# Optimization experiments

Hardware: AMD Instinct MI355X
Metric: run time of the kernel (lower is better)

The kernel has to match this reference:

```python
import jax, jax.numpy as jnp
import numpy as np

N_X = 32640   # total xlmr subword tokens (64 seqs x 510 tokens)
N_S = 16320   # total stanza word tokens (2 subwords per word)
E = 65280     # dependency edges (bidirectional, avg degree ~4)
D = 768
GCN_DIM = 256
GCN_NUM = 2
POS_DIM = 4
N_UPOS = 17
N_LABEL = 5


def setup_inputs() -> dict:
    key = jax.random.key(0)
    ks = jax.random.split(key, 8)
    x = jax.random.normal(ks[0], (N_X, D), dtype=jnp.float32)
    # mapStanza2Xlmr as segment ids: xlmr token j belongs to stanza word j//2
    seg = jnp.arange(N_X, dtype=jnp.int32) // 2
    edge_index = jax.random.randint(ks[1], (2, E), 0, N_S, dtype=jnp.int32)
    upos_ids = jax.random.randint(ks[2], (N_S,), 0, N_UPOS, dtype=jnp.int32)
    Wc = jax.random.normal(ks[3], (D, GCN_DIM), dtype=jnp.float32) * 0.02
    bc = jnp.zeros((GCN_DIM,), dtype=jnp.float32)
    gcn_W = jax.random.normal(ks[4], (GCN_NUM, GCN_DIM, GCN_DIM), dtype=jnp.float32) * 0.05
    gcn_b = jnp.zeros((GCN_NUM, GCN_DIM), dtype=jnp.float32)
    upos_table = jax.random.normal(ks[5], (N_UPOS, POS_DIM), dtype=jnp.float32)
    Wcls = jax.random.normal(ks[6], (D + GCN_DIM + POS_DIM, N_LABEL), dtype=jnp.float32) * 0.02
    bcls = jnp.zeros((N_LABEL,), dtype=jnp.float32)
    return {"x": x, "seg": seg, "edge_index": edge_index, "upos_ids": upos_ids,
            "Wc": Wc, "bc": bc, "gcn_W": gcn_W, "gcn_b": gcn_b,
            "upos_table": upos_table, "Wcls": Wcls, "bcls": bcls}


def _gcn_conv(h, srcs, dsts, W, b, n):
    # PyG GCNConv: h' = D^-1/2 (A+I) D^-1/2 (h W) + b  (self loops already in srcs/dsts)
    h = h @ W
    deg = jax.ops.segment_sum(jnp.ones_like(dsts, h.dtype), dsts, num_segments=n)
    dinv = jax.lax.rsqrt(deg)  # deg >= 1 because of self loops
    coef = dinv[srcs] * dinv[dsts]
    out = jax.ops.segment_sum(h[srcs] * coef[:, None], dsts, num_segments=n)
    return out + b


def reference(x, seg, edge_index, upos_ids, Wc, bc, gcn_W, gcn_b, upos_table, Wcls, bcls):
    # mapStanza2Xlmr: mean-pool subword embeddings into stanza word embeddings
    cnt = jax.ops.segment_sum(jnp.ones((N_X,), x.dtype), seg, num_segments=N_S)
    stanza = jax.ops.segment_sum(x, seg, num_segments=N_S) / cnt[:, None]  # [N_S, D]
    # GCN over dependency edges (gcn_mode=0: biedges)
    h = stanza @ Wc + bc
    self_idx = jnp.arange(N_S, dtype=edge_index.dtype)
    srcs = jnp.concatenate([edge_index[0], self_idx])
    dsts = jnp.concatenate([edge_index[1], self_idx])
    for i in range(GCN_NUM):
        h = jax.nn.relu(_gcn_conv(h, srcs, dsts, gcn_W[i], gcn_b[i], N_S))
    # POS embedding + concat + relu
    pos = upos_table[upos_ids]                                  # [N_S, POS_DIM]
    info = jax.nn.relu(jnp.concatenate([h, pos], axis=1))       # [N_S, GCN_DIM+POS_DIM]
    # mapXlmr2Stanza: each subword gathers its (single) word's info
    append = info[seg]                                          # [N_X, GCN_DIM+POS_DIM]
    tok = jnp.concatenate([x, append], axis=1)                  # [N_X, 1028]
    logits = jax.nn.relu(tok) @ Wcls + bcls
    return jax.nn.log_softmax(logits, axis=1)
```

## Files before the change

### kernel.cpp

```cpp
#include <hip/hip_runtime.h>

#define NXT 32640
#define NS  16320
#define NE  65280
#define DD  768
#define GD  256
#define NLAB 5
#define CAP 32

typedef __attribute__((ext_vector_type(8))) short bf16x8;
typedef __attribute__((ext_vector_type(4))) float f32x4;

__device__ inline unsigned short f2b(float f) {
    unsigned int u = __float_as_uint(f);
    unsigned int r = (u + 0x7FFFu + ((u >> 16) & 1u)) >> 16;
    return (unsigned short)r;
}
__device__ inline float b2f(unsigned short h) {
    return __uint_as_float((unsigned int)h << 16);
}

__global__ void k_setup(int* __restrict__ cnt,
                        const float* __restrict__ Wc, unsigned short* __restrict__ WcT,
                        const float* __restrict__ gcn_W, unsigned short* __restrict__ WT,
                        const float* __restrict__ Wcls, float* __restrict__ WclsT) {
    int b = blockIdx.x, t = threadIdx.x;
    if (b < 64) {
        int i = b * 256 + t;
        if (i < NS) cnt[i] = 0;
    } else if (b < 832) {
        int idx = (b - 64) * 256 + t;
        int k = idx / GD, n = idx - k * GD;
        WcT[(size_t)n * DD + k] = f2b(Wc[idx]);
    } else if (b < 1344) {
        int l = (b < 1088) ? 0 : 1;
        int idx = (b - (l ? 1088 : 832)) * 256 + t;
        int k = idx / GD, n = idx - k * GD;
        WT[(size_t)l * GD * GD + (size_t)n * GD + k] = f2b(gcn_W[(size_t)l * GD * GD + idx]);
    } else {
        int idx = (b - 1344) * 256 + t;
        if (idx < NLAB * DD) {
            int l = idx / DD, k = idx - l * DD;
            WclsT[idx] = Wcls[(size_t)k * NLAB + l];
        }
    }
}

__global__ void k_fill(const int* __restrict__ ei, int* __restrict__ cnt,
                       int* __restrict__ csr_src) {
    int e = blockIdx.x * 256 + threadIdx.x;
    if (e < NE) {
        int dst = ei[NE + e];
        int slot = atomicAdd(&cnt[dst], 1);
        if (slot < CAP) csr_src[(size_t)dst * CAP + slot] = ei[e];
    }
}

__global__ __launch_bounds__(256) void k_xpass(const float* __restrict__ x,
                                               const float* __restrict__ WclsT,
                                               float* __restrict__ partial,
                                               unsigned short* __restrict__ stanza) {
    int w    = blockIdx.x * 4 + (threadIdx.x >> 6);
    int lane = threadIdx.x & 63;
    const float* xr0 = x + (size_t)(2 * w) * DD + lane * 4;
    const float* xr1 = xr0 + DD;
    f32x4 a[3], b[3];
#pragma unroll
    for (int p = 0; p < 3; ++p) {
        a[p] = *(const f32x4*)(xr0 + p * 256);
        b[p] = *(const f32x4*)(xr1 + p * 256);
    }
#pragma unroll
    for (int p = 0; p < 3; ++p) {
        ushort4 o;
        o.x = f2b((a[p][0] + b[p][0]) * 0.5f);
        o.y = f2b((a[p][1] + b[p][1]) * 0.5f);
        o.z = f2b((a[p][2] + b[p][2]) * 0.5f);
        o.w = f2b((a[p][3] + b[p][3]) * 0.5f);
        *(ushort4*)(stanza + (size_t)w * DD + p * 256 + lane * 4) = o;
    }
    f32x4 ra[3], rb[3];
#pragma unroll
    for (int p = 0; p < 3; ++p)
#pragma unroll
        for (int i = 0; i < 4; ++i) {
            ra[p][i] = a[p][i] > 0.f ? a[p][i] : 0.f;
            rb[p][i] = b[p][i] > 0.f ? b[p][i] : 0.f;
        }
    float acc0[NLAB] = {}, acc1[NLAB] = {};
#pragma unroll
    for (int l = 0; l < NLAB; ++l)
#pragma unroll
        for (int p = 0; p < 3; ++p) {
            f32x4 wv = *(const f32x4*)(WclsT + (size_t)l * DD + p * 256 + lane * 4);
#pragma unroll
            for (int i = 0; i < 4; ++i) {
                acc0[l] += ra[p][i] * wv[i];
                acc1[l] += rb[p][i] * wv[i];
            }
        }
#pragma unroll
    for (int off = 32; off > 0; off >>= 1)
#pragma unroll
        for (int l = 0; l < NLAB; ++l) {
            acc0[l] += __shfl_xor(acc0[l], off);
            acc1[l] += __shfl_xor(acc1[l], off);
        }
    if (lane == 0) {
        float* pp = partial + (size_t)w * 2 * NLAB;
#pragma unroll
        for (int l = 0; l < NLAB; ++l) { pp[l] = acc0[l]; pp[NLAB + l] = acc1[l]; }
    }
}

__global__ __launch_bounds__(256) void k_gemm(const unsigned short* __restrict__ A,
                                              const unsigned short* __restrict__ BT,
                                              const float* __restrict__ bias,
                                              unsigned short* __restrict__ out,
                                              int K, int nbn) {
    __shared__ unsigned short lds[(256 + 512) * 8];
    const int tid  = threadIdx.x;
    const int lane = tid & 63;
    const int wv   = tid >> 6;
    const int wr   = wv >> 1, wc = wv & 1;
    const int bm   = (blockIdx.x / nbn) * 64;
    const int bn   = (blockIdx.x % nbn) * 128;

    const int ca = tid;
    const int ga = ca >> 6, wa = ca & 63, kca = wa >> 4, rla = wa & 15;
    const unsigned short* srcA = A + (size_t)(bm + ga * 16 + rla) * K + kca * 8;
    const int cb0 = tid;
    const int gb0 = cb0 >> 6, wb0 = cb0 & 63, kcb0 = wb0 >> 4, rlb0 = wb0 & 15;
    const unsigned short* srcB0 = BT + (size_t)(bn + gb0 * 16 + rlb0) * K + kcb0 * 8;
    const int cb1 = 256 + tid;
    const int gb1 = cb1 >> 6, wb1 = cb1 & 63, kcb1 = wb1 >> 4, rlb1 = wb1 & 15;
    const unsigned short* srcB1 = BT + (size_t)(bn + gb1 * 16 + rlb1) * K + kcb1 * 8;

    unsigned short* dstA  = lds + (size_t)tid * 8;
    unsigned short* dstB0 = lds + (size_t)(256 + tid) * 8;
    unsigned short* dstB1 = lds + (size_t)(512 + tid) * 8;

    const bf16x8* fragA = (const bf16x8*)lds + (wr * 2) * 64 + lane;
    const bf16x8* fragB = (const bf16x8*)lds + 256 + (wc * 4) * 64 + lane;

    f32x4 acc[2][4] = {};
    for (int k0 = 0; k0 < K; k0 += 32) {
        __builtin_amdgcn_global_load_lds(srcA + k0, dstA, 16, 0, 0);
        __builtin_amdgcn_global_load_lds(srcB0 + k0, dstB0, 16, 0, 0);
        __builtin_amdgcn_global_load_lds(srcB1 + k0, dstB1, 16, 0, 0);
        __syncthreads();
        bf16x8 a0 = fragA[0], a1 = fragA[64];
        bf16x8 b0 = fragB[0], b1 = fragB[64], b2 = fragB[128], b3 = fragB[192];
        acc[0][0] = __builtin_amdgcn_mfma_f32_16x16x32_bf16(a0, b0, acc[0][0], 0, 0, 0);
        acc[0][1] = __builtin_amdgcn_mfma_f32_16x16x32_bf16(a0, b1, acc[0][1], 0, 0, 0);
        acc[0][2] = __builtin_amdgcn_mfma_f32_16x16x32_bf16(a0, b2, acc[0][2], 0, 0, 0);
        acc[0][3] = __builtin_amdgcn_mfma_f32_16x16x32_bf16(a0, b3, acc[0][3], 0, 0, 0);
        acc[1][0] = __builtin_amdgcn_mfma_f32_16x16x32_bf16(a1, b0, acc[1][0], 0, 0, 0);
        acc[1][1] = __builtin_amdgcn_mfma_f32_16x16x32_bf16(a1, b1, acc[1][1], 0, 0, 0);
        acc[1][2] = __builtin_amdgcn_mfma_f32_16x16x32_bf16(a1, b2, acc[1][2], 0, 0, 0);
        acc[1][3] = __builtin_amdgcn_mfma_f32_16x16x32_bf16(a1, b3, acc[1][3], 0, 0, 0);
        __syncthreads();
    }

    const int rl = lane & 15, rq = lane >> 4;
#pragma unroll
    for (int m = 0; m < 2; ++m) {
        int row0 = bm + wr * 32 + m * 16 + rq * 4;
#pragma unroll
        for (int n = 0; n < 4; ++n) {
            int col = bn + wc * 64 + n * 16 + rl;
            float bv = bias ? bias[col] : 0.f;
#pragma unroll
            for (int r = 0; r < 4; ++r)
                out[(size_t)(row0 + r) * GD + col] = f2b(acc[m][n][r] + bv);
        }
    }
}

__global__ void k_gather(const int* __restrict__ cnt, const int* __restrict__ csr_src,
                         const unsigned short* __restrict__ hW,
                         const float* __restrict__ b, unsigned short* __restrict__ hout) {
    int w    = blockIdx.x * 4 + (threadIdx.x >> 6);
    int lane = threadIdx.x & 63;
    int c = cnt[w];
    float dw = rsqrtf((float)c + 1.0f);
    const int* sl = csr_src + (size_t)w * CAP;
    float ax = 0.f, ay = 0.f, az = 0.f, aw = 0.f;
    for (int j = 0; j < c; ++j) {
        int src = sl[j];
        float cf = rsqrtf((float)cnt[src] + 1.0f) * dw;
        ushort4 v = *(const ushort4*)&hW[(size_t)src * GD + lane * 4];
        ax += cf * b2f(v.x); ay += cf * b2f(v.y); az += cf * b2f(v.z); aw += cf * b2f(v.w);
    }
    ushort4 sv = *(const ushort4*)&hW[(size_t)w * GD + lane * 4];
    f32x4 bv = *(const f32x4*)&b[lane * 4];
    float c2 = dw * dw;
    float rx = ax + b2f(sv.x) * c2 + bv[0];
    float ry = ay + b2f(sv.y) * c2 + bv[1];
    float rz = az + b2f(sv.z) * c2 + bv[2];
    float rw = aw + b2f(sv.w) * c2 + bv[3];
    ushort4 o;
    o.x = f2b(rx > 0.f ? rx : 0.f);
    o.y = f2b(ry > 0.f ? ry : 0.f);
    o.z = f2b(rz > 0.f ? rz : 0.f);
    o.w = f2b(rw > 0.f ? rw : 0.f);
    *(ushort4*)&hout[(size_t)w * GD + lane * 4] = o;
}

__global__ void k_final(const unsigned short* __restrict__ h, const float* __restrict__ partial,
                        const int* __restrict__ upos_ids,
                        const float* __restrict__ upos_table, const float* __restrict__ Wcls,
                        const float* __restrict__ bcls, float* __restrict__ out) {
    int token = blockIdx.x * 4 + (threadIdx.x >> 6);
    int lane  = threadIdx.x & 63;
    int w = token >> 1;
    ushort4 hv = *(const ushort4*)&h[(size_t)w * GD + lane * 4];
    float vals[4] = {b2f(hv.x), b2f(hv.y), b2f(hv.z), b2f(hv.w)};
    float acc[NLAB] = {};
#pragma unroll
    for (int i = 0; i < 4; ++i) {
        float v = vals[i];
        v = v > 0.f ? v : 0.f;
        const float* wr = Wcls + (size_t)(DD + lane * 4 + i) * NLAB;
#pragma unroll
        for (int l = 0; l < NLAB; ++l) acc[l] += v * wr[l];
    }
#pragma unroll
    for (int off = 32; off > 0; off >>= 1)
#pragma unroll
        for (int l = 0; l < NLAB; ++l) acc[l] += __shfl_down(acc[l], off);
    if (lane == 0) {
        int u = upos_ids[w];
        float lg[NLAB];
#pragma unroll
        for (int l = 0; l < NLAB; ++l) {
            float a = acc[l] + partial[(size_t)token * NLAB + l] + bcls[l];
#pragma unroll
            for (int p = 0; p < 4; ++p) {
                float pv = upos_table[u * 4 + p];
                pv = pv > 0.f ? pv : 0.f;
                a += pv * Wcls[(size_t)(DD + GD + p) * NLAB + l];
            }
            lg[l] = a;
        }
        float m = lg[0];
#pragma unroll
        for (int l = 1; l < NLAB; ++l) m = fmaxf(m, lg[l]);
        float s = 0.f;
#pragma unroll
        for (int l = 0; l < NLAB; ++l) s += __expf(lg[l] - m);
        float lse = __logf(s) + m;
        float* op = out + (size_t)token * NLAB;
#pragma unroll
        for (int l = 0; l < NLAB; ++l) op[l] = lg[l] - lse;
    }
}

extern "C" void kernel_launch(void* const* d_in, const int* in_sizes, int n_in,
                              void* d_out, int out_size, void* d_ws, size_t ws_size,
                              hipStream_t stream) {
    const float* x          = (const float*)d_in[0];
    const int*   ei         = (const int*)d_in[2];
    const int*   upos_ids   = (const int*)d_in[3];
    const float* Wc         = (const float*)d_in[4];
    const float* bc         = (const float*)d_in[5];
    const float* gcn_W      = (const float*)d_in[6];
    const float* gcn_b      = (const float*)d_in[7];
    const float* upos_table = (const float*)d_in[8];
    const float* Wcls       = (const float*)d_in[9];
    const float* bcls       = (const float*)d_in[10];
    float* out = (float*)d_out;

    char* ws = (char*)d_ws;
    float* partial          = (float*)ws;            ws += (size_t)NXT * NLAB * 4;
    float* WclsT            = (float*)ws;            ws += (size_t)NLAB * DD * 4;
    unsigned short* stanza  = (unsigned short*)ws;   ws += (size_t)NS * DD * 2;
    unsigned short* h_bf    = (unsigned short*)ws;   ws += (size_t)NS * GD * 2;
    unsigned short* hW_bf   = (unsigned short*)ws;   ws += (size_t)NS * GD * 2;
    unsigned short* WcT     = (unsigned short*)ws;   ws += (size_t)DD * GD * 2;
    unsigned short* WT      = (unsigned short*)ws;   ws += (size_t)2 * GD * GD * 2;
    int* cnt                = (int*)ws;              ws += (size_t)NS * 4;
    int* csr_src            = (int*)ws;              ws += (size_t)NS * CAP * 4;

    k_setup<<<1359, 256, 0, stream>>>(cnt, Wc, WcT, gcn_W, WT, Wcls, WclsT);
    k_fill<<<(NE + 255) / 256, 256, 0, stream>>>(ei, cnt, csr_src);
    k_xpass<<<NS / 4, 256, 0, stream>>>(x, WclsT, partial, stanza);
    k_gemm<<<(NS / 64) * 2, 256, 0, stream>>>(stanza, WcT, bc, h_bf, DD, 2);
    for (int layer = 0; layer < 2; ++layer) {
        k_gemm<<<(NS / 64) * 2, 256, 0, stream>>>(h_bf, WT + (size_t)layer * GD * GD, nullptr, hW_bf, GD, 2);
        k_gather<<<NS / 4, 256, 0, stream>>>(cnt, csr_src, hW_bf, gcn_b + (size_t)layer * GD, h_bf);
    }
    k_final<<<NXT / 4, 256, 0, stream>>>(h_bf, partial, upos_ids, upos_table, Wcls, bcls, out);
}
```

Baseline: 127.1 us.

## Fuse last GCN gather with classifier head, one wave per word

The second-layer GCN aggregation is merged into the final classifier kernel. Each wave now handles one stanza word and writes log-softmax for both of its subword tokens, which drops the h_bf round trip and halves the per-token h reads and dot products. The POS embedding contribution plus bias is precomputed once per UPOS id into a small table in the setup kernel. The reduction switches to xor shuffles. The fused kernel does more per-wave work and has a divergent edge loop.

```diff
diff --git a/kernel.cpp b/kernel.cpp
--- a/kernel.cpp
+++ b/kernel.cpp
@@ -23,7 +23,9 @@
 __global__ void k_setup(int* __restrict__ cnt,
                         const float* __restrict__ Wc, unsigned short* __restrict__ WcT,
                         const float* __restrict__ gcn_W, unsigned short* __restrict__ WT,
-                        const float* __restrict__ Wcls, float* __restrict__ WclsT) {
+                        const float* __restrict__ Wcls, float* __restrict__ WclsT,
+                        const float* __restrict__ upos_table, const float* __restrict__ bcls,
+                        float* __restrict__ posLogit) {
     int b = blockIdx.x, t = threadIdx.x;
     if (b < 64) {
         int i = b * 256 + t;
@@ -37,11 +39,23 @@
         int idx = (b - (l ? 1088 : 832)) * 256 + t;
         int k = idx / GD, n = idx - k * GD;
         WT[(size_t)l * GD * GD + (size_t)n * GD + k] = f2b(gcn_W[(size_t)l * GD * GD + idx]);
-    } else {
+    } else if (b < 1359) {
         int idx = (b - 1344) * 256 + t;
         if (idx < NLAB * DD) {
             int l = idx / DD, k = idx - l * DD;
             WclsT[idx] = Wcls[(size_t)k * NLAB + l];
+        }
+    } else {
+        if (t < 17 * NLAB) {
+            int u = t / NLAB, l = t - u * NLAB;
+            float a = bcls[l];
+#pragma unroll
+            for (int p = 0; p < 4; ++p) {
+                float pv = upos_table[u * 4 + p];
+                pv = pv > 0.f ? pv : 0.f;
+                a += pv * Wcls[(size_t)(DD + GD + p) * NLAB + l];
+            }
+            posLogit[t] = a;
         }
     }
 }
@@ -207,20 +221,38 @@
     *(ushort4*)&hout[(size_t)w * GD + lane * 4] = o;
 }
 
-__global__ void k_final(const unsigned short* __restrict__ h, const float* __restrict__ partial,
-                        const int* __restrict__ upos_ids,
-                        const float* __restrict__ upos_table, const float* __restrict__ Wcls,
-                        const float* __restrict__ bcls, float* __restrict__ out) {
-    int token = blockIdx.x * 4 + (threadIdx.x >> 6);
-    int lane  = threadIdx.x & 63;
-    int w = token >> 1;
-    ushort4 hv = *(const ushort4*)&h[(size_t)w * GD + lane * 4];
-    float vals[4] = {b2f(hv.x), b2f(hv.y), b2f(hv.z), b2f(hv.w)};
+__global__ void k_gather_final(const int* __restrict__ cnt, const int* __restrict__ csr_src,
+                               const unsigned short* __restrict__ hW,
+                               const float* __restrict__ b,
+                               const float* __restrict__ partial,
+                               const int* __restrict__ upos_ids,
+                               const float* __restrict__ posLogit,
+                               const float* __restrict__ Wcls,
+                               float* __restrict__ out) {
+    int w    = blockIdx.x * 4 + (threadIdx.x >> 6);
+    int lane = threadIdx.x & 63;
+    int c = cnt[w];
+    float dw = rsqrtf((float)c + 1.0f);
+    const int* sl = csr_src + (size_t)w * CAP;
+    float ax = 0.f, ay = 0.f, az = 0.f, aw = 0.f;
+    for (int j = 0; j < c; ++j) {
+        int src = sl[j];
+        float cf = rsqrtf((float)cnt[src] + 1.0f) * dw;
+        ushort4 v = *(const ushort4*)&hW[(size_t)src * GD + lane * 4];
+        ax += cf * b2f(v.x); ay += cf * b2f(v.y); az += cf * b2f(v.z); aw += cf * b2f(v.w);
+    }
+    ushort4 sv = *(const ushort4*)&hW[(size_t)w * GD + lane * 4];
+    f32x4 bv = *(const f32x4*)&b[lane * 4];
+    float c2 = dw * dw;
+    float hv[4];
+    hv[0] = ax + b2f(sv.x) * c2 + bv[0];
+    hv[1] = ay + b2f(sv.y) * c2 + bv[1];
+    hv[2] = az + b2f(sv.z) * c2 + bv[2];
+    hv[3] = aw + b2f(sv.w) * c2 + bv[3];
     float acc[NLAB] = {};
 #pragma unroll
     for (int i = 0; i < 4; ++i) {
-        float v = vals[i];
-        v = v > 0.f ? v : 0.f;
+        float v = hv[i] > 0.f ? hv[i] : 0.f;
         const float* wr = Wcls + (size_t)(DD + lane * 4 + i) * NLAB;
 #pragma unroll
         for (int l = 0; l < NLAB; ++l) acc[l] += v * wr[l];
@@ -228,31 +260,26 @@
 #pragma unroll
     for (int off = 32; off > 0; off >>= 1)
 #pragma unroll
-        for (int l = 0; l < NLAB; ++l) acc[l] += __shfl_down(acc[l], off);
+        for (int l = 0; l < NLAB; ++l) acc[l] += __shfl_xor(acc[l], off);
     if (lane == 0) {
-        int u = upos_ids[w];
-        float lg[NLAB];
-#pragma unroll
-        for (int l = 0; l < NLAB; ++l) {
-            float a = acc[l] + partial[(size_t)token * NLAB + l] + bcls[l];
-#pragma unroll
-            for (int p = 0; p < 4; ++p) {
-                float pv = upos_table[u * 4 + p];
-                pv = pv > 0.f ? pv : 0.f;
-                a += pv * Wcls[(size_t)(DD + GD + p) * NLAB + l];
-            }
-            lg[l] = a;
-        }
-        float m = lg[0];
-#pragma unroll
-        for (int l = 1; l < NLAB; ++l) m = fmaxf(m, lg[l]);
-        float s = 0.f;
-#pragma unroll
-        for (int l = 0; l < NLAB; ++l) s += __expf(lg[l] - m);
-        float lse = __logf(s) + m;
-        float* op = out + (size_t)token * NLAB;
-#pragma unroll
-        for (int l = 0; l < NLAB; ++l) op[l] = lg[l] - lse;
+        const float* pl = posLogit + (size_t)upos_ids[w] * NLAB;
+        const float* pp = partial + (size_t)w * 2 * NLAB;
+#pragma unroll
+        for (int t = 0; t < 2; ++t) {
+            float lg[NLAB];
+#pragma unroll
+            for (int l = 0; l < NLAB; ++l) lg[l] = acc[l] + pp[t * NLAB + l] + pl[l];
+            float m = lg[0];
+#pragma unroll
+            for (int l = 1; l < NLAB; ++l) m = fmaxf(m, lg[l]);
+            float s = 0.f;
+#pragma unroll
+            for (int l = 0; l < NLAB; ++l) s += __expf(lg[l] - m);
+            float lse = __logf(s) + m;
+            float* op = out + (size_t)(2 * w + t) * NLAB;
+#pragma unroll
+            for (int l = 0; l < NLAB; ++l) op[l] = lg[l] - lse;
+        }
     }
 }
 
@@ -274,6 +301,7 @@
     char* ws = (char*)d_ws;
     float* partial          = (float*)ws;            ws += (size_t)NXT * NLAB * 4;
     float* WclsT            = (float*)ws;            ws += (size_t)NLAB * DD * 4;
+    float* posLogit         = (float*)ws;            ws += (size_t)17 * NLAB * 4;
     unsigned short* stanza  = (unsigned short*)ws;   ws += (size_t)NS * DD * 2;
     unsigned short* h_bf    = (unsigned short*)ws;   ws += (size_t)NS * GD * 2;
     unsigned short* hW_bf   = (unsigned short*)ws;   ws += (size_t)NS * GD * 2;
@@ -282,13 +310,14 @@
     int* cnt                = (int*)ws;              ws += (size_t)NS * 4;
     int* csr_src            = (int*)ws;              ws += (size_t)NS * CAP * 4;
 
-    k_setup<<<1359, 256, 0, stream>>>(cnt, Wc, WcT, gcn_W, WT, Wcls, WclsT);
+    k_setup<<<1360, 256, 0, stream>>>(cnt, Wc, WcT, gcn_W, WT, Wcls, WclsT,
+                                      upos_table, bcls, posLogit);
     k_fill<<<(NE + 255) / 256, 256, 0, stream>>>(ei, cnt, csr_src);
     k_xpass<<<NS / 4, 256, 0, stream>>>(x, WclsT, partial, stanza);
     k_gemm<<<(NS / 64) * 2, 256, 0, stream>>>(stanza, WcT, bc, h_bf, DD, 2);
-    for (int layer = 0; layer < 2; ++layer) {
-        k_gemm<<<(NS / 64) * 2, 256, 0, stream>>>(h_bf, WT + (size_t)layer * GD * GD, nullptr, hW_bf, GD, 2);
-        k_gather<<<NS / 4, 256, 0, stream>>>(cnt, csr_src, hW_bf, gcn_b + (size_t)layer * GD, h_bf);
-    }
-    k_final<<<NXT / 4, 256, 0, stream>>>(h_bf, partial, upos_ids, upos_table, Wcls, bcls, out);
-}
+    k_gemm<<<(NS / 64) * 2, 256, 0, stream>>>(h_bf, WT, nullptr, hW_bf, GD, 2);
+    k_gather<<<NS / 4, 256, 0, stream>>>(cnt, csr_src, hW_bf, gcn_b, h_bf);
+    k_gemm<<<(NS / 64) * 2, 256, 0, stream>>>(h_bf, WT + (size_t)GD * GD, nullptr, hW_bf, GD, 2);
+    k_gather_final<<<NS / 4, 256, 0, stream>>>(cnt, csr_src, hW_bf, gcn_b + GD,
+                                               partial, upos_ids, posLogit, Wcls, out);
+}
```

After: 120.7 us. 1.05x faster.
